# Optimization experiments

Measured on AMD Instinct MI355X. Metric: run time of the kernel, lower is better.

## Reference

```python
import jax, jax.numpy as jnp
import numpy as np

B, C, H, W = 32, 64, 56, 56
REPN, NK, SMALL = 50, 17, 3   # repN=64-int(64*0.23), nk=ceil(51/3)
GROUPS = 4                     # N_rep
EPS = 1e-5


def _build_index_mats():
    """Reduce the fallback's python scatter-add loops to exact linear maps.
    For flat position p=r*NK+j the roll shifts depend only on p%3, so each
    shift class s gets a (REPN,NK) count matrix over source nk-slots."""
    rng = np.random.RandomState(123)
    ghost = np.sort(rng.choice(C, C - REPN, replace=False))
    rep = np.array(sorted(set(range(C)) - set(ghost.tolist())), np.int32)
    Mh = np.zeros((3, REPN, NK), np.int32)
    Mv = np.zeros((3, REPN, NK), np.int32)
    Mid = np.zeros((REPN, NK), np.int32)
    for _ in range(GROUPS):
        for r in range(REPN):
            perm = rng.permutation(NK)
            for p in range(NK):
                Mh[(r * NK + p) % 3, r, perm[p]] += 1
        for r in range(REPN):
            perm = rng.permutation(NK)
            for p in range(NK):
                Mv[(r * NK + p) % 3, r, perm[p]] += 1
        kk = rng.randint(0, NK, REPN)
        for r in range(REPN):
            Mid[r, kk[r]] += 1
    return ghost.astype(np.int32), rep, Mh, Mv, Mid


def setup_inputs() -> dict:
    key = jax.random.key(0)
    k1, k2, k3 = jax.random.split(key, 3)
    ghost, rep, Mh, Mv, Mid = _build_index_mats()
    return {
        "inputs": jax.random.normal(k1, (B, C, H, W), jnp.float32),
        "w0": jax.random.normal(k2, (REPN * NK, 1, SMALL, SMALL), jnp.float32) * 0.1,
        "w1": jax.random.normal(k3, (REPN * NK, 1, SMALL, SMALL), jnp.float32) * 0.1,
        "Mh": jnp.asarray(Mh), "Mv": jnp.asarray(Mv), "Mid": jnp.asarray(Mid),
        "ghost_idx": jnp.asarray(ghost), "rep_idx": jnp.asarray(rep),
    }


def _bn(x):
    # BatchNorm2d in training mode, affine weight=1 / bias=0 (init values)
    m = x.mean(axis=(0, 2, 3), keepdims=True)
    v = x.var(axis=(0, 2, 3), keepdims=True)
    return (x - m) / jnp.sqrt(v + EPS)


def reference(inputs, w0, w1, Mh, Mv, Mid, ghost_idx, rep_idx):
    rep_in = inputs[:, rep_idx]      # (B, REPN, H, W)
    ghost_in = inputs[:, ghost_idx]  # (B, ghostN, H, W)

    def conv(w):  # depthwise-grouped conv: groups=REPN, each 1->NK channels
        return jax.lax.conv_general_dilated(
            rep_in, w, window_strides=(1, 1), padding=((2, 2), (2, 2)),
            dimension_numbers=('NCHW', 'OIHW', 'NCHW'),
            feature_group_count=REPN)

    out = conv(w0) + conv(w1)                       # (B, REPN*NK, H+2, W+2)
    xv = out.reshape(B, REPN, NK, H + 2, W + 2)

    Mhf, Mvf, Midf = (m.astype(xv.dtype) for m in (Mh, Mv, Mid))
    sh1, sw1 = (0, 1, 2), (0, 2, 1)   # lora1: shifts (i%3, 2i%3)
    sh2, sw2 = (0, 2, 1), (0, 1, 2)   # lora2: shifts (2i%3, i%3)

    lora1 = sum(jnp.roll(jnp.einsum('rk,brkhw->brhw', Mhf[s], xv),
                         (sh1[s], sw1[s]), axis=(2, 3)) for s in range(3))
    lora2 = sum(jnp.roll(jnp.einsum('rk,brkhw->brhw', Mvf[s], xv),
                         (sh2[s], sw2[s]), axis=(2, 3)) for s in range(3))
    small = jnp.einsum('rk,brkhw->brhw', Midf, xv)

    # center-crop back to (H, W): dh = dw = 1
    lora1 = lora1[:, :, 1:1 + H, 1:1 + W]
    lora2 = lora2[:, :, 1:1 + H, 1:1 + W]
    small = small[:, :, 1:1 + H, 1:1 + W]

    x = _bn(lora1) + _bn(lora2) + _bn(small) + rep_in
    return jnp.concatenate([x, ghost_in], axis=1)   # (B, C, H, W)
```

## Files before the change

### kernel.cpp

```cpp
#include <hip/hip_runtime.h>

#define Bn 32
#define Cn 64
#define Hn 56
#define Wn 56
#define REPN 50
#define NKn 17
#define HWn (Hn*Wn)
#define NSTATf 100352.0f
#define EPSf 1e-5f

#define TSTR 68
#define TROWS 60
#define TSZ (TROWS*TSTR)

#define NQ 784

#define PLANE (Bn*REPN*HWn)
#define L1_OFF 0
#define L2_OFF PLANE
#define SM_OFF (2*PLANE)
#define PART_OFF (3*PLANE)

__device__ __forceinline__ void conv_quad(const float* __restrict__ tile,
        const float* __restrict__ wk, int g,
        float* __restrict__ l1, float* __restrict__ l2,
        float* __restrict__ sm, float* __restrict__ res)
{
    int h  = g / 14;
    int wq = g - h*14;
    int w0 = wq * 4;
    bool topwrap = (h == 0);
    #pragma unroll
    for (int p = 0; p < 4; ++p) { l1[p]=0.f; l2[p]=0.f; sm[p]=0.f; }

    {
        int row = topwrap ? 57 : (h-1);
        const float* rp = tile + row*TSTR + w0;
        float4 qa = *(const float4*)rp;
        float4 qb = *(const float4*)(rp+4);
        float X[8] = {qa.x,qa.y,qa.z,qa.w,qb.x,qb.y,qb.z,qb.w};
        #pragma unroll
        for (int p = 0; p < 4; ++p)
            #pragma unroll
            for (int j = 0; j < 3; ++j) {
                float v = X[2+p+j];
                l1[p] = fmaf(v, wk[18+j], l1[p]);
                l2[p] = fmaf(v, wk[36+j], l2[p]);
            }
    }
    #pragma unroll
    for (int d = 0; d < 4; ++d) {
        const float* rp = tile + (h+d)*TSTR + w0;
        float4 qa = *(const float4*)rp;
        float4 qb = *(const float4*)(rp+4);
        float X[9] = {qa.x,qa.y,qa.z,qa.w,qb.x,qb.y,qb.z,qb.w,0.f};
        if (d >= 1) X[8] = rp[8];
        if (d == 2) { res[0]=X[4]; res[1]=X[5]; res[2]=X[6]; res[3]=X[7]; }
        if (d <= 1) {
            #pragma unroll
            for (int p = 0; p < 4; ++p)
                #pragma unroll
                for (int j = 0; j < 3; ++j) {
                    float v = topwrap ? 0.f : X[2+p+j];
                    l1[p] = fmaf(v, wk[21+3*d+j], l1[p]);
                    l2[p] = fmaf(v, wk[39+3*d+j], l2[p]);
                }
        }
        if (d <= 2) {
            #pragma unroll
            for (int p = 0; p < 4; ++p)
                #pragma unroll
                for (int j = 0; j < 3; ++j) {
                    float v = X[1+p+j];
                    l1[p] = fmaf(v, wk[9+3*d+j],  l1[p]);
                    l2[p] = fmaf(v, wk[45+3*d+j], l2[p]);
                }
        }
        if (d >= 1) {
            #pragma unroll
            for (int p = 0; p < 4; ++p)
                #pragma unroll
                for (int j = 0; j < 3; ++j) {
                    float v = X[3+p+j];
                    l1[p] = fmaf(v, wk[3*(d-1)+j],    l1[p]);
                    l2[p] = fmaf(v, wk[27+3*(d-1)+j], l2[p]);
                    sm[p] = fmaf(v, wk[54+3*(d-1)+j], sm[p]);
                }
        }
    }
    if (wq == 0) {
        #pragma unroll
        for (int d = 0; d < 3; ++d) {
            float v = tile[(h+d)*TSTR + 59];
            l1[0] = fmaf(v, wk[9+3*d],  l1[0]);
            l2[0] = fmaf(v, wk[45+3*d], l2[0]);
        }
    }
}

__global__ void __launch_bounds__(256) k_conv(const float* __restrict__ in,
        const float* __restrict__ w0g, const float* __restrict__ w1g,
        const int* __restrict__ Mh, const int* __restrict__ Mv,
        const int* __restrict__ Mid, const int* __restrict__ rep_idx,
        float* __restrict__ ws)
{
    __shared__ __align__(16) float tile[TSZ];
    __shared__ float wkl[63];
    __shared__ float red[4][6];
    int bid = blockIdx.x;
    int r = bid % REPN;
    int b = bid / REPN;
    int tid = threadIdx.x;
    int cin = rep_idx[r];

    if (tid < 63) {
        int t  = tid / 9;
        int ij = tid % 9;
        const int* M = (t < 3) ? (Mh + (t*REPN + r)*NKn)
                     : (t < 6) ? (Mv + ((t-3)*REPN + r)*NKn)
                               : (Mid + r*NKn);
        float acc = 0.f;
        #pragma unroll
        for (int k = 0; k < NKn; ++k) {
            int m = M[k];
            acc += (float)m * (w0g[(r*NKn + k)*9 + ij] + w1g[(r*NKn + k)*9 + ij]);
        }
        wkl[tid] = acc;
    }
    for (int i = tid; i < TSZ/4; i += 256) *(float4*)(tile + 4*i) = make_float4(0,0,0,0);
    __syncthreads();
    const float4* s4 = (const float4*)(in + ((size_t)(b*Cn + cin))*HWn);
    for (int i = tid; i < HWn/4; i += 256) {
        float4 v = s4[i];
        int e = i * 4;
        int row = e / Wn;
        int col = e % Wn;
        *(float4*)(tile + (2 + row)*TSTR + 4 + col) = v;
    }
    __syncthreads();

    float wk[63];
    #pragma unroll
    for (int i = 0; i < 63; ++i) wk[i] = wkl[i];

    size_t base = (size_t)(b*REPN + r)*HWn;
    float4* p1 = (float4*)(ws + L1_OFF + base);
    float4* p2 = (float4*)(ws + L2_OFF + base);
    float4* p3 = (float4*)(ws + SM_OFF + base);

    float s1=0.f,q1=0.f,s2=0.f,q2=0.f,s3=0.f,q3=0.f;
    for (int g = tid; g < NQ; g += 256) {
        float l1[4], l2[4], sm[4], res[4];
        conv_quad(tile, wk, g, l1, l2, sm, res);
        p1[g] = make_float4(l1[0],l1[1],l1[2],l1[3]);
        p2[g] = make_float4(l2[0],l2[1],l2[2],l2[3]);
        p3[g] = make_float4(sm[0],sm[1],sm[2],sm[3]);
        #pragma unroll
        for (int p = 0; p < 4; ++p) {
            s1 += l1[p]; q1 += l1[p]*l1[p];
            s2 += l2[p]; q2 += l2[p]*l2[p];
            s3 += sm[p]; q3 += sm[p]*sm[p];
        }
    }
    float vals[6] = {s1,q1,s2,q2,s3,q3};
    int lane = tid & 63, wave = tid >> 6;
    #pragma unroll
    for (int q = 0; q < 6; ++q) {
        float v = vals[q];
        for (int o = 32; o; o >>= 1) v += __shfl_down(v, o, 64);
        if (lane == 0) red[wave][q] = v;
    }
    __syncthreads();
    if (tid < 6)
        ws[PART_OFF + (tid*REPN + r)*Bn + b] =
            red[0][tid] + red[1][tid] + red[2][tid] + red[3][tid];
}

__global__ void __launch_bounds__(256) k_final(const float* __restrict__ in,
        const int* __restrict__ rep_idx, const int* __restrict__ ghost_idx,
        const float* __restrict__ ws, float* __restrict__ out)
{
    int bid = blockIdx.x;
    int c = bid % Cn;
    int b = bid / Cn;
    int tid = threadIdx.x;

    if (c >= REPN) {
        int cin = ghost_idx[c - REPN];
        const float4* s4 = (const float4*)(in + ((size_t)(b*Cn + cin))*HWn);
        float4* d4 = (float4*)(out + ((size_t)(b*Cn + c))*HWn);
        for (int i = tid; i < HWn/4; i += 256) d4[i] = s4[i];
        return;
    }

    __shared__ float sred[6];
    int r = c;
    if (tid < 6) {
        const float* pp = ws + PART_OFF + (tid*REPN + r)*Bn;
        float s = 0.f;
        #pragma unroll
        for (int i = 0; i < Bn; ++i) s += pp[i];
        sred[tid] = s;
    }
    __syncthreads();
    const float inv = 1.0f / NSTATf;
    float m1 = sred[0]*inv, v1 = sred[1]*inv - m1*m1;
    float m2 = sred[2]*inv, v2 = sred[3]*inv - m2*m2;
    float m3 = sred[4]*inv, v3 = sred[5]*inv - m3*m3;
    float r1 = rsqrtf(v1 + EPSf), r2 = rsqrtf(v2 + EPSf), r3 = rsqrtf(v3 + EPSf);

    int cin = rep_idx[r];
    size_t base = (size_t)(b*REPN + r)*HWn;
    const float4* p1 = (const float4*)(ws + L1_OFF + base);
    const float4* p2 = (const float4*)(ws + L2_OFF + base);
    const float4* p3 = (const float4*)(ws + SM_OFF + base);
    const float4* rin = (const float4*)(in + ((size_t)(b*Cn + cin))*HWn);
    float4* d4 = (float4*)(out + ((size_t)(b*Cn + c))*HWn);

    for (int i = tid; i < HWn/4; i += 256) {
        float4 a = p1[i], d = p2[i], e = p3[i], x = rin[i];
        float4 o;
        o.x = (a.x-m1)*r1 + (d.x-m2)*r2 + (e.x-m3)*r3 + x.x;
        o.y = (a.y-m1)*r1 + (d.y-m2)*r2 + (e.y-m3)*r3 + x.y;
        o.z = (a.z-m1)*r1 + (d.z-m2)*r2 + (e.z-m3)*r3 + x.z;
        o.w = (a.w-m1)*r1 + (d.w-m2)*r2 + (e.w-m3)*r3 + x.w;
        d4[i] = o;
    }
}

extern "C" void kernel_launch(void* const* d_in, const int* in_sizes, int n_in,
                              void* d_out, int out_size, void* d_ws, size_t ws_size,
                              hipStream_t stream) {
    const float* in   = (const float*)d_in[0];
    const float* w0   = (const float*)d_in[1];
    const float* w1   = (const float*)d_in[2];
    const int*   Mh   = (const int*)d_in[3];
    const int*   Mv   = (const int*)d_in[4];
    const int*   Mid  = (const int*)d_in[5];
    const int*   ghost= (const int*)d_in[6];
    const int*   rep  = (const int*)d_in[7];
    float* out  = (float*)d_out;
    float* ws   = (float*)d_ws;

    k_conv<<<Bn*REPN, 256, 0, stream>>>(in, w0, w1, Mh, Mv, Mid, rep, ws);
    k_final<<<Bn*Cn, 256, 0, stream>>>(in, rep, ghost, ws, out);
}
```

Baseline: 136.0 us.

## Replace LDS tile conv with register sliding-window rows and precomputed effective weights

Moves the per-block effective-weight reduction into a separate small kernel that writes 63 weights per channel to workspace. The conv kernel drops the shared-memory tile and reads rows straight from global memory. Each thread keeps a 5-row sliding register window over a 7-row segment, with 112 active threads out of 128 per block. This removes the LDS fill, zeroing and barriers, but adds register pressure, repeated global/L2 reads of overlapping columns, and leaves 16 threads idle per block.

```diff
diff --git a/kernel.cpp b/kernel.cpp
--- a/kernel.cpp
+++ b/kernel.cpp
@@ -10,171 +10,174 @@
 #define NSTATf 100352.0f
 #define EPSf 1e-5f
 
-#define TSTR 68
-#define TROWS 60
-#define TSZ (TROWS*TSTR)
-
-#define NQ 784
-
 #define PLANE (Bn*REPN*HWn)
 #define L1_OFF 0
 #define L2_OFF PLANE
 #define SM_OFF (2*PLANE)
 #define PART_OFF (3*PLANE)
-
-__device__ __forceinline__ void conv_quad(const float* __restrict__ tile,
-        const float* __restrict__ wk, int g,
-        float* __restrict__ l1, float* __restrict__ l2,
-        float* __restrict__ sm, float* __restrict__ res)
-{
-    int h  = g / 14;
-    int wq = g - h*14;
-    int w0 = wq * 4;
-    bool topwrap = (h == 0);
+#define WEFF_OFF (3*PLANE + 9600)
+
+#define SEGH 7
+#define SEGS 8
+#define NTASK (SEGS*14)
+
+__global__ void k_weff(const float* __restrict__ w0, const float* __restrict__ w1,
+                       const int* __restrict__ Mh, const int* __restrict__ Mv,
+                       const int* __restrict__ Mid, float* __restrict__ ws)
+{
+    int idx = blockIdx.x * blockDim.x + threadIdx.x;
+    if (idx >= REPN*63) return;
+    int r   = idx / 63;
+    int rem = idx % 63;
+    int t   = rem / 9;
+    int ij  = rem % 9;
+    const int* M = (t < 3) ? (Mh + (t*REPN + r)*NKn)
+                 : (t < 6) ? (Mv + ((t-3)*REPN + r)*NKn)
+                           : (Mid + r*NKn);
+    float acc = 0.f;
     #pragma unroll
-    for (int p = 0; p < 4; ++p) { l1[p]=0.f; l2[p]=0.f; sm[p]=0.f; }
-
-    {
-        int row = topwrap ? 57 : (h-1);
-        const float* rp = tile + row*TSTR + w0;
-        float4 qa = *(const float4*)rp;
-        float4 qb = *(const float4*)(rp+4);
-        float X[8] = {qa.x,qa.y,qa.z,qa.w,qb.x,qb.y,qb.z,qb.w};
-        #pragma unroll
-        for (int p = 0; p < 4; ++p)
-            #pragma unroll
-            for (int j = 0; j < 3; ++j) {
-                float v = X[2+p+j];
-                l1[p] = fmaf(v, wk[18+j], l1[p]);
-                l2[p] = fmaf(v, wk[36+j], l2[p]);
-            }
-    }
-    #pragma unroll
-    for (int d = 0; d < 4; ++d) {
-        const float* rp = tile + (h+d)*TSTR + w0;
-        float4 qa = *(const float4*)rp;
-        float4 qb = *(const float4*)(rp+4);
-        float X[9] = {qa.x,qa.y,qa.z,qa.w,qb.x,qb.y,qb.z,qb.w,0.f};
-        if (d >= 1) X[8] = rp[8];
-        if (d == 2) { res[0]=X[4]; res[1]=X[5]; res[2]=X[6]; res[3]=X[7]; }
-        if (d <= 1) {
-            #pragma unroll
-            for (int p = 0; p < 4; ++p)
-                #pragma unroll
-                for (int j = 0; j < 3; ++j) {
-                    float v = topwrap ? 0.f : X[2+p+j];
-                    l1[p] = fmaf(v, wk[21+3*d+j], l1[p]);
-                    l2[p] = fmaf(v, wk[39+3*d+j], l2[p]);
-                }
-        }
-        if (d <= 2) {
-            #pragma unroll
-            for (int p = 0; p < 4; ++p)
-                #pragma unroll
-                for (int j = 0; j < 3; ++j) {
-                    float v = X[1+p+j];
-                    l1[p] = fmaf(v, wk[9+3*d+j],  l1[p]);
-                    l2[p] = fmaf(v, wk[45+3*d+j], l2[p]);
-                }
-        }
-        if (d >= 1) {
-            #pragma unroll
-            for (int p = 0; p < 4; ++p)
-                #pragma unroll
-                for (int j = 0; j < 3; ++j) {
-                    float v = X[3+p+j];
-                    l1[p] = fmaf(v, wk[3*(d-1)+j],    l1[p]);
-                    l2[p] = fmaf(v, wk[27+3*(d-1)+j], l2[p]);
-                    sm[p] = fmaf(v, wk[54+3*(d-1)+j], sm[p]);
-                }
-        }
-    }
-    if (wq == 0) {
-        #pragma unroll
-        for (int d = 0; d < 3; ++d) {
-            float v = tile[(h+d)*TSTR + 59];
-            l1[0] = fmaf(v, wk[9+3*d],  l1[0]);
-            l2[0] = fmaf(v, wk[45+3*d], l2[0]);
-        }
-    }
-}
-
-__global__ void __launch_bounds__(256) k_conv(const float* __restrict__ in,
-        const float* __restrict__ w0g, const float* __restrict__ w1g,
-        const int* __restrict__ Mh, const int* __restrict__ Mv,
-        const int* __restrict__ Mid, const int* __restrict__ rep_idx,
-        float* __restrict__ ws)
-{
-    __shared__ __align__(16) float tile[TSZ];
-    __shared__ float wkl[63];
-    __shared__ float red[4][6];
+    for (int k = 0; k < NKn; ++k)
+        acc += (float)M[k] * (w0[(r*NKn + k)*9 + ij] + w1[(r*NKn + k)*9 + ij]);
+    ws[WEFF_OFF + idx] = acc;
+}
+
+__device__ __forceinline__ void load_row8c(const float* __restrict__ ch, int row, int q,
+                                           float* __restrict__ X, float& c55)
+{
+    bool rv = (row >= 0) && (row < Hn);
+    int rc = rv ? row : 0;
+    const float* rp = ch + rc*Wn;
+    float4 c0 = *(const float4*)(rp + (q ? 4*q - 4 : 0));
+    float4 c1 = *(const float4*)(rp + 4*q);
+    int ox = (4*q + 4 <= 55) ? 4*q + 4 : 55;
+    float cx = rp[ox];
+    float mr = rv ? 1.f : 0.f;
+    float m0 = (rv && q > 0)  ? 1.f : 0.f;
+    float mx = (rv && q < 13) ? 1.f : 0.f;
+    X[0]=c0.y*m0; X[1]=c0.z*m0; X[2]=c0.w*m0;
+    X[3]=c1.x*mr; X[4]=c1.y*mr; X[5]=c1.z*mr; X[6]=c1.w*mr;
+    X[7]=cx*mx;
+    c55 = (q == 0) ? rp[55]*mr : 0.f;
+}
+
+__global__ void __launch_bounds__(128) k_conv(const float* __restrict__ in,
+        const int* __restrict__ rep_idx, float* __restrict__ ws)
+{
     int bid = blockIdx.x;
     int r = bid % REPN;
     int b = bid / REPN;
     int tid = threadIdx.x;
-    int cin = rep_idx[r];
-
-    if (tid < 63) {
-        int t  = tid / 9;
-        int ij = tid % 9;
-        const int* M = (t < 3) ? (Mh + (t*REPN + r)*NKn)
-                     : (t < 6) ? (Mv + ((t-3)*REPN + r)*NKn)
-                               : (Mid + r*NKn);
-        float acc = 0.f;
-        #pragma unroll
-        for (int k = 0; k < NKn; ++k) {
-            int m = M[k];
-            acc += (float)m * (w0g[(r*NKn + k)*9 + ij] + w1g[(r*NKn + k)*9 + ij]);
-        }
-        wkl[tid] = acc;
-    }
-    for (int i = tid; i < TSZ/4; i += 256) *(float4*)(tile + 4*i) = make_float4(0,0,0,0);
-    __syncthreads();
-    const float4* s4 = (const float4*)(in + ((size_t)(b*Cn + cin))*HWn);
-    for (int i = tid; i < HWn/4; i += 256) {
-        float4 v = s4[i];
-        int e = i * 4;
-        int row = e / Wn;
-        int col = e % Wn;
-        *(float4*)(tile + (2 + row)*TSTR + 4 + col) = v;
-    }
-    __syncthreads();
-
+
+    const float* wr = ws + WEFF_OFF + r*63;
     float wk[63];
     #pragma unroll
-    for (int i = 0; i < 63; ++i) wk[i] = wkl[i];
-
-    size_t base = (size_t)(b*REPN + r)*HWn;
-    float4* p1 = (float4*)(ws + L1_OFF + base);
-    float4* p2 = (float4*)(ws + L2_OFF + base);
-    float4* p3 = (float4*)(ws + SM_OFF + base);
+    for (int i = 0; i < 63; ++i) wk[i] = wr[i];
+
+    int cin = rep_idx[r];
+    const float* ch = in + ((size_t)(b*Cn + cin))*HWn;
 
     float s1=0.f,q1=0.f,s2=0.f,q2=0.f,s3=0.f,q3=0.f;
-    for (int g = tid; g < NQ; g += 256) {
-        float l1[4], l2[4], sm[4], res[4];
-        conv_quad(tile, wk, g, l1, l2, sm, res);
-        p1[g] = make_float4(l1[0],l1[1],l1[2],l1[3]);
-        p2[g] = make_float4(l2[0],l2[1],l2[2],l2[3]);
-        p3[g] = make_float4(sm[0],sm[1],sm[2],sm[3]);
+
+    if (tid < NTASK) {
+        int seg = tid / 14;
+        int q   = tid - seg*14;
+        int h0  = seg * SEGH;
+        bool top = (seg == 0);
+
+        float W[5][8], C[5], T[8];
+        {
+            float dummy;
+            if (top) load_row8c(ch, 55, q, T, dummy);
+        }
         #pragma unroll
-        for (int p = 0; p < 4; ++p) {
-            s1 += l1[p]; q1 += l1[p]*l1[p];
-            s2 += l2[p]; q2 += l2[p]*l2[p];
-            s3 += sm[p]; q3 += sm[p]*sm[p];
+        for (int k = 0; k < 5; ++k)
+            load_row8c(ch, h0 - 3 + k, q, W[k], C[k]);
+
+        size_t base = ((size_t)(b*REPN + r))*HWn;
+        float* p1 = ws + L1_OFF + base;
+        float* p2 = ws + L2_OFF + base;
+        float* p3 = ws + SM_OFF + base;
+
+        #pragma unroll
+        for (int s = 0; s < SEGH; ++s) {
+            int h = h0 + s;
+            float Wn8[8], Cn1;
+            load_row8c(ch, h + 2, q, Wn8, Cn1);
+
+            float l1[4], l2[4], sm[4];
+            #pragma unroll
+            for (int p = 0; p < 4; ++p) { l1[p]=0.f; l2[p]=0.f; sm[p]=0.f; }
+            #pragma unroll
+            for (int i = 0; i < 3; ++i)
+                #pragma unroll
+                for (int j = 0; j < 3; ++j) {
+                    float wh0 = wk[i*3+j],    wv0 = wk[27+i*3+j], wid = wk[54+i*3+j];
+                    float wh1 = wk[9+i*3+j],  wv2 = wk[45+i*3+j];
+                    float wh2 = wk[18+i*3+j], wv1 = wk[36+i*3+j];
+                    #pragma unroll
+                    for (int p = 0; p < 4; ++p) {
+                        float a  = W[2+i][p+2+j];
+                        l1[p] = fmaf(a, wh0, l1[p]);
+                        l2[p] = fmaf(a, wv0, l2[p]);
+                        sm[p] = fmaf(a, wid, sm[p]);
+                        float bA = W[1+i][p+j];
+                        l1[p] = fmaf(bA, wh1, l1[p]);
+                        l2[p] = fmaf(bA, wv2, l2[p]);
+                        float bB = W[i][p+1+j];
+                        l1[p] = fmaf(bB, wh2, l1[p]);
+                        l2[p] = fmaf(bB, wv1, l2[p]);
+                    }
+                }
+            if (q == 0) {
+                #pragma unroll
+                for (int i = 0; i < 3; ++i) {
+                    l1[0] = fmaf(C[1+i], wk[9+3*i],  l1[0]);
+                    l2[0] = fmaf(C[1+i], wk[45+3*i], l2[0]);
+                }
+            }
+            if (s == 0 && top) {
+                #pragma unroll
+                for (int j = 0; j < 3; ++j)
+                    #pragma unroll
+                    for (int p = 0; p < 4; ++p) {
+                        l1[p] = fmaf(T[p+1+j], wk[18+j], l1[p]);
+                        l2[p] = fmaf(T[p+1+j], wk[36+j], l2[p]);
+                    }
+            }
+            int o = h*Wn + 4*q;
+            *(float4*)(p1 + o) = make_float4(l1[0],l1[1],l1[2],l1[3]);
+            *(float4*)(p2 + o) = make_float4(l2[0],l2[1],l2[2],l2[3]);
+            *(float4*)(p3 + o) = make_float4(sm[0],sm[1],sm[2],sm[3]);
+            #pragma unroll
+            for (int p = 0; p < 4; ++p) {
+                s1 += l1[p]; q1 += l1[p]*l1[p];
+                s2 += l2[p]; q2 += l2[p]*l2[p];
+                s3 += sm[p]; q3 += sm[p]*sm[p];
+            }
+            #pragma unroll
+            for (int k = 0; k < 4; ++k) {
+                #pragma unroll
+                for (int x = 0; x < 8; ++x) W[k][x] = W[k+1][x];
+                C[k] = C[k+1];
+            }
+            #pragma unroll
+            for (int x = 0; x < 8; ++x) W[4][x] = Wn8[x];
+            C[4] = Cn1;
         }
     }
+
+    __shared__ float red[2][6];
     float vals[6] = {s1,q1,s2,q2,s3,q3};
     int lane = tid & 63, wave = tid >> 6;
     #pragma unroll
-    for (int q = 0; q < 6; ++q) {
-        float v = vals[q];
-        for (int o = 32; o; o >>= 1) v += __shfl_down(v, o, 64);
-        if (lane == 0) red[wave][q] = v;
+    for (int v = 0; v < 6; ++v) {
+        float x = vals[v];
+        for (int o = 32; o; o >>= 1) x += __shfl_down(x, o, 64);
+        if (lane == 0) red[wave][v] = x;
     }
     __syncthreads();
     if (tid < 6)
-        ws[PART_OFF + (tid*REPN + r)*Bn + b] =
-            red[0][tid] + red[1][tid] + red[2][tid] + red[3][tid];
+        ws[PART_OFF + (tid*REPN + r)*Bn + b] = red[0][tid] + red[1][tid];
 }
 
 __global__ void __launch_bounds__(256) k_final(const float* __restrict__ in,
@@ -243,6 +246,7 @@
     float* out  = (float*)d_out;
     float* ws   = (float*)d_ws;
 
-    k_conv<<<Bn*REPN, 256, 0, stream>>>(in, w0, w1, Mh, Mv, Mid, rep, ws);
+    k_weff<<<(REPN*63 + 255)/256, 256, 0, stream>>>(w0, w1, Mh, Mv, Mid, ws);
+    k_conv<<<Bn*REPN, 128, 0, stream>>>(in, rep, ws);
     k_final<<<Bn*Cn, 256, 0, stream>>>(in, rep, ghost, ws, out);
 }
```

After: 125.0 us. 1.09x faster.
